# Kernel tuning notes

Measured on AMD Instinct MI355X. Metric: run time of the kernel, lower is better.

Reference implementation:

```python
import jax, jax.numpy as jnp
import numpy as np

B, IN, OUT = 8192, 512, 1024

def setup_inputs() -> dict:
    key = jax.random.key(0)
    k1, k2 = jax.random.split(key)
    return {
        "input": jax.random.normal(k1, (B, IN), dtype=jnp.float32),
        "centres": jax.random.normal(k2, (OUT, IN), dtype=jnp.float32),
        "log_sigmas": jnp.zeros((OUT,), dtype=jnp.float32),
    }

def reference(input, centres, log_sigmas):
    x_sq = jnp.sum(input * input, axis=-1, keepdims=True)          # [B, 1]
    c_sq = jnp.sum(centres * centres, axis=-1)                     # [OUT]
    cross = input @ centres.T                                      # [B, OUT] GEMM
    d2 = jnp.maximum(x_sq - 2.0 * cross + c_sq[None, :], 0.0)
    distances = jnp.sqrt(d2) / jnp.exp(log_sigmas)[None, :]        # [B, OUT]
    # gaussian basis function: phi(alpha) = exp(-alpha^2)
    return jnp.exp(-(distances * distances))
```

## Files before the change

### kernel.cpp

```cpp
#include <hip/hip_runtime.h>
#include <hip/hip_bf16.h>


#define B_ROWS 8192
#define IN_K   512
#define OUT_N  1024
#define BK     64
#define NKT    (IN_K / BK)

typedef __attribute__((ext_vector_type(8))) __bf16 bf16x8;
typedef __attribute__((ext_vector_type(4))) __bf16 bf16x4;
typedef __attribute__((ext_vector_type(4))) float  floatx4;

__device__ __forceinline__ void gload_lds16(const void* g, void* l) {
    __builtin_amdgcn_global_load_lds((const __attribute__((address_space(1))) void*)g,
                                     (__attribute__((address_space(3))) void*)l,
                                     16, 0, 0);
}

__global__ __launch_bounds__(256) void convert_sumsq(
    const float* __restrict__ X, const float* __restrict__ C,
    __bf16* __restrict__ Xbf, __bf16* __restrict__ Cbf,
    float* __restrict__ xsq, float* __restrict__ csq)
{
    int wid  = (blockIdx.x * 256 + threadIdx.x) >> 6;
    int lane = threadIdx.x & 63;
    const float* src; __bf16* dst; float* sq;
    if (wid < B_ROWS) {
        src = X + (size_t)wid * IN_K; dst = Xbf + (size_t)wid * IN_K; sq = xsq + wid;
    } else {
        int r = wid - B_ROWS;
        src = C + (size_t)r * IN_K;  dst = Cbf + (size_t)r * IN_K;  sq = csq + r;
    }
    const float4* s4 = reinterpret_cast<const float4*>(src);
    float4 a = s4[lane];
    float4 b = s4[lane + 64];
    bf16x4 va = {(__bf16)a.x, (__bf16)a.y, (__bf16)a.z, (__bf16)a.w};
    bf16x4 vb = {(__bf16)b.x, (__bf16)b.y, (__bf16)b.z, (__bf16)b.w};
    *reinterpret_cast<bf16x4*>(dst + lane * 4)       = va;
    *reinterpret_cast<bf16x4*>(dst + 256 + lane * 4) = vb;
    float s = a.x*a.x + a.y*a.y + a.z*a.z + a.w*a.w
            + b.x*b.x + b.y*b.y + b.z*b.z + b.w*b.w;
    #pragma unroll
    for (int off = 32; off; off >>= 1) s += __shfl_xor(s, off, 64);
    if (lane == 0) *sq = s;
}

__global__ __launch_bounds__(256, 2) void rbf_gemm(
    const __bf16* __restrict__ Xbf,
    const __bf16* __restrict__ Cbf,
    const float* __restrict__ LS,
    const float* __restrict__ xsq,
    const float* __restrict__ csq,
    float* __restrict__ out)
{
    __shared__ __bf16 As[2][128 * BK];
    __shared__ __bf16 Bs[2][128 * BK];

    const int tid  = threadIdx.x;
    const int sid  = blockIdx.x;
    const int bidx = (sid & 7) * 64 + (sid >> 3);
    const int bm   = bidx >> 3;
    const int bn   = bidx & 7;
    const int brow = bm * 128;
    const int bcol = bn * 128;
    const int lane = tid & 63;
    const int w    = tid >> 6;
    const int wr   = w >> 1;
    const int wc   = w & 1;
    const int l15  = lane & 15;
    const int l4   = lane >> 4;

    const int srow = tid >> 3;
    const int col8 = (((tid & 7) ^ (srow & 7)) * 8);
    const __bf16* Asrc = Xbf + (size_t)(brow + srow) * IN_K + col8;
    const __bf16* Bsrc = Cbf + (size_t)(bcol + srow) * IN_K + col8;

    auto stage = [&](int kt, int buf) {
        #pragma unroll
        for (int i = 0; i < 4; ++i)
            gload_lds16(Asrc + (size_t)i * 32 * IN_K + kt * BK, &As[buf][tid * 8 + i * 2048]);
        #pragma unroll
        for (int i = 0; i < 4; ++i)
            gload_lds16(Bsrc + (size_t)i * 32 * IN_K + kt * BK, &Bs[buf][tid * 8 + i * 2048]);
    };

    floatx4 acc[4][4];
    #pragma unroll
    for (int m = 0; m < 4; ++m)
        #pragma unroll
        for (int n = 0; n < 4; ++n)
            acc[m][n] = (floatx4){0.f, 0.f, 0.f, 0.f};

    stage(0, 0);

    #pragma unroll 1
    for (int kt = 0; kt < NKT; ++kt) {
        const int cur = kt & 1;
        __syncthreads();
        if (kt < NKT - 1) stage(kt + 1, cur ^ 1);

        #pragma unroll
        for (int ks = 0; ks < 2; ++ks) {
            bf16x8 af[4], bfr[4];
            #pragma unroll
            for (int m = 0; m < 4; ++m) {
                int r = wr * 64 + m * 16 + l15;
                int kslot = l4 + ks * 4;
                af[m] = *reinterpret_cast<const bf16x8*>(
                    &As[cur][r * BK + ((kslot ^ (r & 7)) * 8)]);
            }
            #pragma unroll
            for (int n = 0; n < 4; ++n) {
                int r = wc * 64 + n * 16 + l15;
                int kslot = l4 + ks * 4;
                bfr[n] = *reinterpret_cast<const bf16x8*>(
                    &Bs[cur][r * BK + ((kslot ^ (r & 7)) * 8)]);
            }
            #pragma unroll
            for (int m = 0; m < 4; ++m)
                #pragma unroll
                for (int n = 0; n < 4; ++n)
                    acc[m][n] = __builtin_amdgcn_mfma_f32_16x16x32_bf16(af[m], bfr[n], acc[m][n], 0, 0, 0);
        }
    }

    float xs[4][4];
    #pragma unroll
    for (int m = 0; m < 4; ++m) {
        int row0 = brow + wr * 64 + m * 16 + l4 * 4;
        #pragma unroll
        for (int r = 0; r < 4; ++r) xs[m][r] = xsq[row0 + r];
    }

    #pragma unroll
    for (int n = 0; n < 4; ++n) {
        int col   = bcol + wc * 64 + n * 16 + l15;
        float cs  = csq[col];
        float inv = __expf(-2.f * LS[col]);
        #pragma unroll
        for (int m = 0; m < 4; ++m) {
            int row0 = brow + wr * 64 + m * 16 + l4 * 4;
            #pragma unroll
            for (int r = 0; r < 4; ++r) {
                float cross = acc[m][n][r];
                float d2 = fmaxf(xs[m][r] + cs - 2.f * cross, 0.f);
                out[(size_t)(row0 + r) * OUT_N + col] = __expf(-d2 * inv);
            }
        }
    }
}

extern "C" void kernel_launch(void* const* d_in, const int* in_sizes, int n_in,
                              void* d_out, int out_size, void* d_ws, size_t ws_size,
                              hipStream_t stream) {
    const float* X  = (const float*)d_in[0];
    const float* C  = (const float*)d_in[1];
    const float* LS = (const float*)d_in[2];
    float* out = (float*)d_out;

    float*  xsq = (float*)d_ws;
    float*  csq = (float*)((char*)d_ws + 32768);
    __bf16* Xbf = (__bf16*)((char*)d_ws + 65536);
    __bf16* Cbf = (__bf16*)((char*)d_ws + 65536 + (size_t)B_ROWS * IN_K * 2);

    convert_sumsq<<<(B_ROWS + OUT_N) / 4, 256, 0, stream>>>(X, C, Xbf, Cbf, xsq, csq);
    rbf_gemm<<<(B_ROWS / 128) * (OUT_N / 128), 256, 0, stream>>>(Xbf, Cbf, LS, xsq, csq, out);
}
```

Measured before the change: 88.14 us.

## Fuse fp32-to-bf16 conversion and squared norms into the GEMM kernel

Removes the separate convert_sumsq pre-pass and its bf16 workspace round-trip. The GEMM now loads fp32 tiles of X and C into registers, accumulates the squared norms, converts to bf16 and stores into a swizzled LDS layout. BK is halved to 32 and occupancy is raised to three blocks per SM. The trade-off is that each block reads fp32 X and C directly (twice the bytes of bf16) and recomputes the conversion and norms redundantly: every X row is redone by all 8 column blocks and every C row by all 64 row blocks. The async direct-to-LDS loads are replaced by register staging.

```diff
diff --git a/kernel.cpp b/kernel.cpp
--- a/kernel.cpp
+++ b/kernel.cpp
@@ -5,57 +5,23 @@
 #define B_ROWS 8192
 #define IN_K   512
 #define OUT_N  1024
-#define BK     64
+#define BK     32
 #define NKT    (IN_K / BK)
 
 typedef __attribute__((ext_vector_type(8))) __bf16 bf16x8;
 typedef __attribute__((ext_vector_type(4))) __bf16 bf16x4;
 typedef __attribute__((ext_vector_type(4))) float  floatx4;
 
-__device__ __forceinline__ void gload_lds16(const void* g, void* l) {
-    __builtin_amdgcn_global_load_lds((const __attribute__((address_space(1))) void*)g,
-                                     (__attribute__((address_space(3))) void*)l,
-                                     16, 0, 0);
-}
-
-__global__ __launch_bounds__(256) void convert_sumsq(
-    const float* __restrict__ X, const float* __restrict__ C,
-    __bf16* __restrict__ Xbf, __bf16* __restrict__ Cbf,
-    float* __restrict__ xsq, float* __restrict__ csq)
-{
-    int wid  = (blockIdx.x * 256 + threadIdx.x) >> 6;
-    int lane = threadIdx.x & 63;
-    const float* src; __bf16* dst; float* sq;
-    if (wid < B_ROWS) {
-        src = X + (size_t)wid * IN_K; dst = Xbf + (size_t)wid * IN_K; sq = xsq + wid;
-    } else {
-        int r = wid - B_ROWS;
-        src = C + (size_t)r * IN_K;  dst = Cbf + (size_t)r * IN_K;  sq = csq + r;
-    }
-    const float4* s4 = reinterpret_cast<const float4*>(src);
-    float4 a = s4[lane];
-    float4 b = s4[lane + 64];
-    bf16x4 va = {(__bf16)a.x, (__bf16)a.y, (__bf16)a.z, (__bf16)a.w};
-    bf16x4 vb = {(__bf16)b.x, (__bf16)b.y, (__bf16)b.z, (__bf16)b.w};
-    *reinterpret_cast<bf16x4*>(dst + lane * 4)       = va;
-    *reinterpret_cast<bf16x4*>(dst + 256 + lane * 4) = vb;
-    float s = a.x*a.x + a.y*a.y + a.z*a.z + a.w*a.w
-            + b.x*b.x + b.y*b.y + b.z*b.z + b.w*b.w;
-    #pragma unroll
-    for (int off = 32; off; off >>= 1) s += __shfl_xor(s, off, 64);
-    if (lane == 0) *sq = s;
-}
-
-__global__ __launch_bounds__(256, 2) void rbf_gemm(
-    const __bf16* __restrict__ Xbf,
-    const __bf16* __restrict__ Cbf,
+__global__ __launch_bounds__(256, 3) void rbf_fused(
+    const float* __restrict__ X,
+    const float* __restrict__ C,
     const float* __restrict__ LS,
-    const float* __restrict__ xsq,
-    const float* __restrict__ csq,
     float* __restrict__ out)
 {
     __shared__ __bf16 As[2][128 * BK];
     __shared__ __bf16 Bs[2][128 * BK];
+    __shared__ float  xsq_s[128];
+    __shared__ float  csq_s[128];
 
     const int tid  = threadIdx.x;
     const int sid  = blockIdx.x;
@@ -71,18 +37,34 @@
     const int l15  = lane & 15;
     const int l4   = lane >> 4;
 
-    const int srow = tid >> 3;
-    const int col8 = (((tid & 7) ^ (srow & 7)) * 8);
-    const __bf16* Asrc = Xbf + (size_t)(brow + srow) * IN_K + col8;
-    const __bf16* Bsrc = Cbf + (size_t)(bcol + srow) * IN_K + col8;
+    const int sq  = tid & 7;
+    const int sr0 = tid >> 3;
+    const float* Asrc = X + (size_t)(brow + sr0) * IN_K + sq * 4;
+    const float* Bsrc = C + (size_t)(bcol + sr0) * IN_K + sq * 4;
+    const int wofs = sr0 * 32 + (((sq >> 1) ^ ((sr0 >> 1) & 3)) * 8) + (sq & 1) * 4;
 
-    auto stage = [&](int kt, int buf) {
+    float4 ar[4], br[4];
+    float  xa[4] = {0.f, 0.f, 0.f, 0.f};
+    float  ca[4] = {0.f, 0.f, 0.f, 0.f};
+
+    auto load = [&](int kt) {
         #pragma unroll
-        for (int i = 0; i < 4; ++i)
-            gload_lds16(Asrc + (size_t)i * 32 * IN_K + kt * BK, &As[buf][tid * 8 + i * 2048]);
+        for (int i = 0; i < 4; ++i) {
+            ar[i] = *reinterpret_cast<const float4*>(Asrc + (size_t)i * 32 * IN_K + kt * BK);
+            br[i] = *reinterpret_cast<const float4*>(Bsrc + (size_t)i * 32 * IN_K + kt * BK);
+        }
+    };
+    auto procstore = [&](int buf) {
         #pragma unroll
-        for (int i = 0; i < 4; ++i)
-            gload_lds16(Bsrc + (size_t)i * 32 * IN_K + kt * BK, &Bs[buf][tid * 8 + i * 2048]);
+        for (int i = 0; i < 4; ++i) {
+            float4 a = ar[i], b = br[i];
+            xa[i] += a.x*a.x + a.y*a.y + a.z*a.z + a.w*a.w;
+            ca[i] += b.x*b.x + b.y*b.y + b.z*b.z + b.w*b.w;
+            bf16x4 va = {(__bf16)a.x, (__bf16)a.y, (__bf16)a.z, (__bf16)a.w};
+            bf16x4 vb = {(__bf16)b.x, (__bf16)b.y, (__bf16)b.z, (__bf16)b.w};
+            *reinterpret_cast<bf16x4*>(&As[buf][wofs + i * 1024]) = va;
+            *reinterpret_cast<bf16x4*>(&Bs[buf][wofs + i * 1024]) = vb;
+        }
     };
 
     floatx4 acc[4][4];
@@ -92,60 +74,74 @@
         for (int n = 0; n < 4; ++n)
             acc[m][n] = (floatx4){0.f, 0.f, 0.f, 0.f};
 
-    stage(0, 0);
+    load(0);
+    procstore(0);
 
     #pragma unroll 1
     for (int kt = 0; kt < NKT; ++kt) {
         const int cur = kt & 1;
         __syncthreads();
-        if (kt < NKT - 1) stage(kt + 1, cur ^ 1);
+        if (kt < NKT - 1) load(kt + 1);
 
+        bf16x8 af[4], bfr[4];
         #pragma unroll
-        for (int ks = 0; ks < 2; ++ks) {
-            bf16x8 af[4], bfr[4];
+        for (int m = 0; m < 4; ++m) {
+            int rr   = wr * 64 + m * 16 + l15;
+            int phys = l4 ^ ((rr >> 1) & 3);
+            af[m] = *reinterpret_cast<const bf16x8*>(&As[cur][rr * 32 + phys * 8]);
+        }
+        #pragma unroll
+        for (int n = 0; n < 4; ++n) {
+            int rr   = wc * 64 + n * 16 + l15;
+            int phys = l4 ^ ((rr >> 1) & 3);
+            bfr[n] = *reinterpret_cast<const bf16x8*>(&Bs[cur][rr * 32 + phys * 8]);
+        }
+        #pragma unroll
+        for (int m = 0; m < 4; ++m)
             #pragma unroll
-            for (int m = 0; m < 4; ++m) {
-                int r = wr * 64 + m * 16 + l15;
-                int kslot = l4 + ks * 4;
-                af[m] = *reinterpret_cast<const bf16x8*>(
-                    &As[cur][r * BK + ((kslot ^ (r & 7)) * 8)]);
-            }
-            #pragma unroll
-            for (int n = 0; n < 4; ++n) {
-                int r = wc * 64 + n * 16 + l15;
-                int kslot = l4 + ks * 4;
-                bfr[n] = *reinterpret_cast<const bf16x8*>(
-                    &Bs[cur][r * BK + ((kslot ^ (r & 7)) * 8)]);
-            }
-            #pragma unroll
-            for (int m = 0; m < 4; ++m)
-                #pragma unroll
-                for (int n = 0; n < 4; ++n)
-                    acc[m][n] = __builtin_amdgcn_mfma_f32_16x16x32_bf16(af[m], bfr[n], acc[m][n], 0, 0, 0);
+            for (int n = 0; n < 4; ++n)
+                acc[m][n] = __builtin_amdgcn_mfma_f32_16x16x32_bf16(af[m], bfr[n], acc[m][n], 0, 0, 0);
+
+        if (kt < NKT - 1) procstore(cur ^ 1);
+    }
+
+    #pragma unroll
+    for (int i = 0; i < 4; ++i) {
+        #pragma unroll
+        for (int off = 1; off <= 4; off <<= 1) {
+            xa[i] += __shfl_xor(xa[i], off, 64);
+            ca[i] += __shfl_xor(ca[i], off, 64);
         }
     }
+    if ((tid & 7) == 0) {
+        #pragma unroll
+        for (int i = 0; i < 4; ++i) {
+            xsq_s[sr0 + 32 * i] = xa[i];
+            csq_s[sr0 + 32 * i] = ca[i];
+        }
+    }
+    __syncthreads();
 
     float xs[4][4];
     #pragma unroll
     for (int m = 0; m < 4; ++m) {
-        int row0 = brow + wr * 64 + m * 16 + l4 * 4;
+        int r0l = wr * 64 + m * 16 + l4 * 4;
         #pragma unroll
-        for (int r = 0; r < 4; ++r) xs[m][r] = xsq[row0 + r];
+        for (int r = 0; r < 4; ++r) xs[m][r] = xsq_s[r0l + r];
     }
 
     #pragma unroll
     for (int n = 0; n < 4; ++n) {
-        int col   = bcol + wc * 64 + n * 16 + l15;
-        float cs  = csq[col];
-        float inv = __expf(-2.f * LS[col]);
+        int cl    = wc * 64 + n * 16 + l15;
+        float cs  = csq_s[cl];
+        float inv = __expf(-2.f * LS[bcol + cl]);
         #pragma unroll
         for (int m = 0; m < 4; ++m) {
-            int row0 = brow + wr * 64 + m * 16 + l4 * 4;
+            int r0 = brow + wr * 64 + m * 16 + l4 * 4;
             #pragma unroll
             for (int r = 0; r < 4; ++r) {
-                float cross = acc[m][n][r];
-                float d2 = fmaxf(xs[m][r] + cs - 2.f * cross, 0.f);
-                out[(size_t)(row0 + r) * OUT_N + col] = __expf(-d2 * inv);
+                float d2 = fmaxf(xs[m][r] + cs - 2.f * acc[m][n][r], 0.f);
+                out[(size_t)(r0 + r) * OUT_N + bcol + cl] = __expf(-d2 * inv);
             }
         }
     }
@@ -159,11 +155,5 @@
     const float* LS = (const float*)d_in[2];
     float* out = (float*)d_out;
 
-    float*  xsq = (float*)d_ws;
-    float*  csq = (float*)((char*)d_ws + 32768);
-    __bf16* Xbf = (__bf16*)((char*)d_ws + 65536);
-    __bf16* Cbf = (__bf16*)((char*)d_ws + 65536 + (size_t)B_ROWS * IN_K * 2);
-
-    convert_sumsq<<<(B_ROWS + OUT_N) / 4, 256, 0, stream>>>(X, C, Xbf, Cbf, xsq, csq);
-    rbf_gemm<<<(B_ROWS / 128) * (OUT_N / 128), 256, 0, stream>>>(Xbf, Cbf, LS, xsq, csq, out);
+    rbf_fused<<<(B_ROWS / 128) * (OUT_N / 128), 256, 0, stream>>>(X, C, LS, out);
 }
```

Measured after the change: 99.51 us. 12.9% more time.

## Use 4-stage LDS pipeline with BK=32 and manual vmcnt waits

Applied to the files above, without the earlier changes.

Halves the K tile to 32 and moves from a double-buffered LDS ring to a 4-buffer ring with three tiles prefetched ahead. The __syncthreads is replaced by a raw s_barrier plus explicit s_waitcnt vmcnt counts and sched_barriers. The swizzle is adjusted to suit the 64-byte rows. The aim is to hide global-load latency better and reduce barrier stalls, at the cost of more iterations, more barriers per K, and a hand-managed wait protocol that could race if the counts are wrong. The launch_bounds occupancy hint of 2 is dropped.

```diff
diff --git a/kernel.cpp b/kernel.cpp
--- a/kernel.cpp
+++ b/kernel.cpp
@@ -5,7 +5,7 @@
 #define B_ROWS 8192
 #define IN_K   512
 #define OUT_N  1024
-#define BK     64
+#define BK     32
 #define NKT    (IN_K / BK)
 
 typedef __attribute__((ext_vector_type(8))) __bf16 bf16x8;
@@ -46,16 +46,13 @@
     if (lane == 0) *sq = s;
 }
 
-__global__ __launch_bounds__(256, 2) void rbf_gemm(
-    const __bf16* __restrict__ Xbf,
-    const __bf16* __restrict__ Cbf,
-    const float* __restrict__ LS,
-    const float* __restrict__ xsq,
-    const float* __restrict__ csq,
-    float* __restrict__ out)
+__global__ __launch_bounds__(256) void rbf_gemm3(
+    const __bf16* __restrict__ Xbf, const __bf16* __restrict__ Cbf,
+    const float* __restrict__ LS, const float* __restrict__ xsq,
+    const float* __restrict__ csq, float* __restrict__ out)
 {
-    __shared__ __bf16 As[2][128 * BK];
-    __shared__ __bf16 Bs[2][128 * BK];
+    __shared__ __align__(16) __bf16 As[4][128 * BK];
+    __shared__ __align__(16) __bf16 Bs[4][128 * BK];
 
     const int tid  = threadIdx.x;
     const int sid  = blockIdx.x;
@@ -71,18 +68,18 @@
     const int l15  = lane & 15;
     const int l4   = lane >> 4;
 
-    const int srow = tid >> 3;
-    const int col8 = (((tid & 7) ^ (srow & 7)) * 8);
-    const __bf16* Asrc = Xbf + (size_t)(brow + srow) * IN_K + col8;
-    const __bf16* Bsrc = Cbf + (size_t)(bcol + srow) * IN_K + col8;
+    const int srow = tid >> 2;
+    const int ksl  = (((tid & 3) ^ ((srow >> 1) & 3)) * 8);
+    const __bf16* Asrc = Xbf + (size_t)(brow + srow) * IN_K + ksl;
+    const __bf16* Bsrc = Cbf + (size_t)(bcol + srow) * IN_K + ksl;
 
     auto stage = [&](int kt, int buf) {
         #pragma unroll
-        for (int i = 0; i < 4; ++i)
-            gload_lds16(Asrc + (size_t)i * 32 * IN_K + kt * BK, &As[buf][tid * 8 + i * 2048]);
+        for (int i = 0; i < 2; ++i)
+            gload_lds16(Asrc + (size_t)i * 64 * IN_K + kt * BK, &As[buf][tid * 8 + i * 2048]);
         #pragma unroll
-        for (int i = 0; i < 4; ++i)
-            gload_lds16(Bsrc + (size_t)i * 32 * IN_K + kt * BK, &Bs[buf][tid * 8 + i * 2048]);
+        for (int i = 0; i < 2; ++i)
+            gload_lds16(Bsrc + (size_t)i * 64 * IN_K + kt * BK, &Bs[buf][tid * 8 + i * 2048]);
     };
 
     floatx4 acc[4][4];
@@ -93,36 +90,45 @@
             acc[m][n] = (floatx4){0.f, 0.f, 0.f, 0.f};
 
     stage(0, 0);
+    stage(1, 1);
+    stage(2, 2);
+    asm volatile("s_waitcnt vmcnt(8)" ::: "memory");
 
     #pragma unroll 1
     for (int kt = 0; kt < NKT; ++kt) {
-        const int cur = kt & 1;
-        __syncthreads();
-        if (kt < NKT - 1) stage(kt + 1, cur ^ 1);
+        const int cur = kt & 3;
+        __builtin_amdgcn_s_barrier();
+        __builtin_amdgcn_sched_barrier(0);
 
+        bf16x8 af[4], bfr[4];
         #pragma unroll
-        for (int ks = 0; ks < 2; ++ks) {
-            bf16x8 af[4], bfr[4];
+        for (int m = 0; m < 4; ++m) {
+            int rr = wr * 64 + m * 16 + l15;
+            af[m] = *reinterpret_cast<const bf16x8*>(
+                &As[cur][rr * BK + ((l4 ^ ((rr >> 1) & 3)) * 8)]);
+        }
+        #pragma unroll
+        for (int n = 0; n < 4; ++n) {
+            int rr = wc * 64 + n * 16 + l15;
+            bfr[n] = *reinterpret_cast<const bf16x8*>(
+                &Bs[cur][rr * BK + ((l4 ^ ((rr >> 1) & 3)) * 8)]);
+        }
+        #pragma unroll
+        for (int m = 0; m < 4; ++m)
             #pragma unroll
-            for (int m = 0; m < 4; ++m) {
-                int r = wr * 64 + m * 16 + l15;
-                int kslot = l4 + ks * 4;
-                af[m] = *reinterpret_cast<const bf16x8*>(
-                    &As[cur][r * BK + ((kslot ^ (r & 7)) * 8)]);
-            }
-            #pragma unroll
-            for (int n = 0; n < 4; ++n) {
-                int r = wc * 64 + n * 16 + l15;
-                int kslot = l4 + ks * 4;
-                bfr[n] = *reinterpret_cast<const bf16x8*>(
-                    &Bs[cur][r * BK + ((kslot ^ (r & 7)) * 8)]);
-            }
-            #pragma unroll
-            for (int m = 0; m < 4; ++m)
-                #pragma unroll
-                for (int n = 0; n < 4; ++n)
-                    acc[m][n] = __builtin_amdgcn_mfma_f32_16x16x32_bf16(af[m], bfr[n], acc[m][n], 0, 0, 0);
+            for (int n = 0; n < 4; ++n)
+                acc[m][n] = __builtin_amdgcn_mfma_f32_16x16x32_bf16(af[m], bfr[n], acc[m][n], 0, 0, 0);
+
+        if (kt + 3 < NKT) {
+            stage(kt + 3, (kt + 3) & 3);
+            __builtin_amdgcn_sched_barrier(0);
+            asm volatile("s_waitcnt vmcnt(8)" ::: "memory");
+        } else if (kt + 2 < NKT) {
+            asm volatile("s_waitcnt vmcnt(4)" ::: "memory");
+        } else if (kt + 1 < NKT) {
+            asm volatile("s_waitcnt vmcnt(0)" ::: "memory");
         }
+        __builtin_amdgcn_sched_barrier(0);
     }
 
     float xs[4][4];
@@ -143,8 +149,7 @@
             int row0 = brow + wr * 64 + m * 16 + l4 * 4;
             #pragma unroll
             for (int r = 0; r < 4; ++r) {
-                float cross = acc[m][n][r];
-                float d2 = fmaxf(xs[m][r] + cs - 2.f * cross, 0.f);
+                float d2 = fmaxf(xs[m][r] + cs - 2.f * acc[m][n][r], 0.f);
                 out[(size_t)(row0 + r) * OUT_N + col] = __expf(-d2 * inv);
             }
         }
@@ -165,5 +170,5 @@
     __bf16* Cbf = (__bf16*)((char*)d_ws + 65536 + (size_t)B_ROWS * IN_K * 2);
 
     convert_sumsq<<<(B_ROWS + OUT_N) / 4, 256, 0, stream>>>(X, C, Xbf, Cbf, xsq, csq);
-    rbf_gemm<<<(B_ROWS / 128) * (OUT_N / 128), 256, 0, stream>>>(Xbf, Cbf, LS, xsq, csq, out);
+    rbf_gemm3<<<(B_ROWS / 128) * (OUT_N / 128), 256, 0, stream>>>(Xbf, Cbf, LS, xsq, csq, out);
 }
```

Measured after the change: 92.64 us. 1.05x slower.
